# Kernel tuning notes

Measured on AMD Instinct MI355X. Metric: run time of the kernel, lower is better.

The kernel has to match this reference:

```python
import jax, jax.numpy as jnp
import numpy as np

NUM_HEADS = 8
WS = 8          # window_size
MO = 12         # (1 + overlap) * window_size
PAD = 2         # overlap * window_size / 2


def setup_inputs() -> dict:
    key = jax.random.key(0)
    ks = jax.random.split(key, 5)
    B, C, H, W = 16, 256, 64, 64
    x = jax.random.normal(ks[0], (B, C, H, W), jnp.float32)
    W1 = jax.random.normal(ks[1], (3 * C, C), jnp.float32) * 0.02
    b1 = jnp.zeros((3 * C,), jnp.float32)
    W2 = jax.random.normal(ks[2], (C, C), jnp.float32) * 0.02
    b2 = jnp.zeros((C,), jnp.float32)
    return {"x": x, "W1": W1, "b1": b1, "W2": W2, "b2": b2}


def _unfold_windows(t, nwin):
    # t: (B, H, W, C) -> overlapping windows (B, nH, nwin, nwin, MO*MO, E)
    # Matches torch nn.Unfold(kernel=MO, stride=WS, padding=PAD) layout:
    # channels outermost, then kernel rows, then kernel cols.
    B, H, W, C = t.shape
    E = C // NUM_HEADS
    p = jnp.pad(t.transpose(0, 3, 1, 2), ((0, 0), (0, 0), (PAD, PAD), (PAD, PAD)))
    idx = (jnp.arange(nwin) * WS)[:, None] + jnp.arange(MO)  # (nwin, MO)
    g = p[:, :, idx]            # (B, C, nwin, MO, Wp)
    g = g[:, :, :, :, idx]      # (B, C, nwin, MO, nwin, MO)
    g = g.transpose(0, 1, 2, 4, 3, 5)            # (B, C, nwin, nwin, MO, MO)
    g = g.reshape(B, NUM_HEADS, E, nwin, nwin, MO * MO)
    return g.transpose(0, 1, 3, 4, 5, 2)         # (B, nH, nwin, nwin, MO^2, E)


def reference(x, W1, b1, W2, b2):
    B, C, H, W = x.shape
    E = C // NUM_HEADS
    nwin = H // WS
    t = x.transpose(0, 2, 3, 1)                  # (B, H, W, C)
    qkv = t @ W1.T + b1                          # (B, H, W, 3C)
    # '(c K)' layout with K=3: channel index outer, K inner -> strided split
    Q = qkv[..., 0::3]
    K = qkv[..., 1::3]
    V = qkv[..., 2::3]
    # Q -> non-overlapping windows: (B, nH, nwin, nwin, WS^2, E)
    Qw = Q.reshape(B, nwin, WS, nwin, WS, NUM_HEADS, E)
    Qw = Qw.transpose(0, 5, 1, 3, 2, 4, 6).reshape(B, NUM_HEADS, nwin, nwin, WS * WS, E)
    Kw = _unfold_windows(K, nwin)
    Vw = _unfold_windows(V, nwin)
    scale = 1.0 / jnp.sqrt(jnp.float32(E))
    scores = jnp.einsum('bhijqe,bhijke->bhijqk', Qw, Kw) * scale  # (B,nH,nw,nw,WS^2,MO^2)
    A = jax.nn.softmax(scores, axis=-1)
    out = jnp.einsum('bhijqk,bhijke->bhijqe', A, Vw)              # (B,nH,nw,nw,WS^2,E)
    out = out.reshape(B, NUM_HEADS, nwin, nwin, WS, WS, E)
    out = out.transpose(0, 2, 4, 3, 5, 1, 6).reshape(B, H, W, C)
    y = out @ W2.T + b2                                           # (B, H, W, C)
    return y.transpose(0, 3, 1, 2)                                # (B, C, H, W)
```

## Files before the change

kernel.cpp:

```cpp
#include <hip/hip_runtime.h>
#include <stdint.h>

typedef unsigned short u16;
typedef unsigned int   u32;
typedef __bf16 bf16x8_t __attribute__((ext_vector_type(8)));
typedef float  f32x4_t  __attribute__((ext_vector_type(4)));

#define MFMA16(a, b, c) __builtin_amdgcn_mfma_f32_16x16x32_bf16((a), (b), (c), 0, 0, 0)

__device__ __forceinline__ float bf2f(u16 u) {
    union { u32 i; float f; } c; c.i = ((u32)u) << 16; return c.f;
}
__device__ __forceinline__ u16 f2bf(float f) {
    union { float f; u32 i; } c; c.f = f;
    u32 x = c.i;
    return (u16)((x + 0x7fffu + ((x >> 16) & 1u)) >> 16);
}
__device__ __forceinline__ u32 cvtpk(float lo, float hi) {
    u32 r;
    asm("v_cvt_pk_bf16_f32 %0, %1, %2" : "=v"(r) : "v"(lo), "v"(hi));
    return r;
}
__device__ __forceinline__ float exp2g(float x) {
    return __builtin_amdgcn_exp2f(x);
}

typedef const unsigned int __attribute__((address_space(1)))* gas_t;
typedef unsigned int __attribute__((address_space(3)))* las_t;
__device__ __forceinline__ void gload16(const u16* g, const u16* l) {
    __builtin_amdgcn_global_load_lds((gas_t)(const void*)g, (las_t)(void*)l, 16, 0, 0);
}

__device__ __forceinline__ u32 detect_fp32(const u16* __restrict__ xu,
                                           int tid, int* wcnt) {
    u16 w = xu[2 * tid];
    int e = (w >> 7) & 0xff;
    int ok = (e >= 80 && e <= 160) ? 1 : 0;
    unsigned long long m = __ballot(ok);
    if ((tid & 63) == 0) wcnt[tid >> 6] = __popcll(m);
    __syncthreads();
    int cnt = wcnt[0] + wcnt[1] + wcnt[2] + wcnt[3];
    return (cnt < 160) ? 1u : 0u;
}

__global__ __launch_bounds__(256) void conv_w(const u16* __restrict__ xu,
                                              const void* __restrict__ W1,
                                              const void* __restrict__ b1,
                                              const void* __restrict__ W2,
                                              const void* __restrict__ b2,
                                              u16* __restrict__ W1b,
                                              u16* __restrict__ b1b,
                                              u16* __restrict__ W2b,
                                              u16* __restrict__ b2b) {
    __shared__ int wcnt[4];
    u32 f = detect_fp32(xu, threadIdx.x, wcnt);
    int i = blockIdx.x * 256 + threadIdx.x;
    const int n1 = 196608, n2 = 768, n3 = 65536;
    if (i < n1) {
        int o = i >> 8, col = i & 255;
        int h = o / 96, rem = o - h * 96;
        int w = rem >> 5, e = rem & 31;
        int src = (3 * (h * 32 + e) + w) * 256 + col;
        W1b[i] = f ? f2bf(((const float*)W1)[src]) : ((const u16*)W1)[src];
    } else if (i < n1 + n2) {
        int o = i - n1;
        int h = o / 96, rem = o - h * 96;
        int w = rem >> 5, e = rem & 31;
        int src = 3 * (h * 32 + e) + w;
        b1b[o] = f ? f2bf(((const float*)b1)[src]) : ((const u16*)b1)[src];
    } else if (i < n1 + n2 + n3) {
        int li = i - n1 - n2;
        W2b[li] = f ? f2bf(((const float*)W2)[li]) : ((const u16*)W2)[li];
    } else {
        int li = i - n1 - n2 - n3;
        b2b[li] = f ? f2bf(((const float*)b2)[li]) : ((const u16*)b2)[li];
    }
}

__global__ __launch_bounds__(256) void conv_x(const void* __restrict__ X,
                                              u16* __restrict__ XT) {
    __shared__ __align__(16) u16 tile[64][68];
    __shared__ int wcnt[4];
    const int tid = threadIdx.x;
    u32 f = detect_fp32((const u16*)X, tid, wcnt);
    const int b = blockIdx.z, c0 = blockIdx.y * 64, h0 = blockIdx.x * 64;
    const int col = tid & 63, rq = tid >> 6;
    if (f) {
        const float* Xf = (const float*)X;
#pragma unroll
        for (int i = 0; i < 16; i++) {
            int row = i * 4 + rq;
            tile[row][col] = f2bf(Xf[((size_t)(b * 256 + c0 + row)) * 4096 + h0 + col]);
        }
    } else {
        const u16* Xh = (const u16*)X;
#pragma unroll
        for (int i = 0; i < 16; i++) {
            int row = i * 4 + rq;
            tile[row][col] = Xh[((size_t)(b * 256 + c0 + row)) * 4096 + h0 + col];
        }
    }
    __syncthreads();
#pragma unroll
    for (int i = 0; i < 16; i++) {
        int row = i * 4 + rq;
        XT[((size_t)(b * 4096 + h0 + row)) * 256 + c0 + col] = tile[col][row];
    }
}

__global__ __launch_bounds__(256) void gemm_qkv(const u16* __restrict__ XT,
                                                const u16* __restrict__ W1,
                                                const u16* __restrict__ b1,
                                                u16* __restrict__ Q2,
                                                u16* __restrict__ K2,
                                                u16* __restrict__ V2) {
    __shared__ __align__(16) u16 smem[128 * 64 + 96 * 64];
    u16* sA = smem;
    u16* sB = smem + 128 * 64;
    u16* Cs = smem;

    const int tid  = threadIdx.x;
    const int lane = tid & 63, wave = tid >> 6;
    const int quad = lane >> 4, l16 = lane & 15;
    const int wm = wave * 32;
    const int bx = blockIdx.x;
    const int bm = (bx >> 6) * 8 + (bx & 7);
    const int h  = (bx >> 3) & 7;
    const int o_base = h * 96;

    f32x4_t acc[2][6];
    const f32x4_t zz = {0.f, 0.f, 0.f, 0.f};
#pragma unroll
    for (int i = 0; i < 2; i++)
#pragma unroll
        for (int j = 0; j < 6; j++) acc[i][j] = zz;

    const int sub = lane >> 3;
    const int cpw = (lane & 7) ^ sub;
    const u16* gA[4]; const u16* gB[3];
    const u16* lA[4]; const u16* lB[3];
#pragma unroll
    for (int i = 0; i < 4; i++) {
        int r8 = (wave * 4 + i) * 8;
        gA[i] = XT + ((size_t)(bm * 128 + r8 + sub)) * 256 + cpw * 8;
        lA[i] = sA + r8 * 64;
    }
#pragma unroll
    for (int i = 0; i < 3; i++) {
        int r8 = (wave * 3 + i) * 8;
        gB[i] = W1 + ((size_t)(o_base + r8 + sub)) * 256 + cpw * 8;
        lB[i] = sB + r8 * 64;
    }

    for (int kt = 0; kt < 256; kt += 64) {
        __syncthreads();
#pragma unroll
        for (int i = 0; i < 4; i++) gload16(gA[i] + kt, lA[i]);
#pragma unroll
        for (int i = 0; i < 3; i++) gload16(gB[i] + kt, lB[i]);
        __syncthreads();
#pragma unroll
        for (int ks = 0; ks < 2; ks++) {
            bf16x8_t af[2], bg[6];
#pragma unroll
            for (int i = 0; i < 2; i++) {
                int row = wm + i * 16 + l16;
                int cp = (ks * 4 + quad) ^ (row & 7);
                af[i] = *(const bf16x8_t*)(sA + row * 64 + cp * 8);
            }
#pragma unroll
            for (int j = 0; j < 6; j++) {
                int row = j * 16 + l16;
                int cp = (ks * 4 + quad) ^ (row & 7);
                bg[j] = *(const bf16x8_t*)(sB + row * 64 + cp * 8);
            }
#pragma unroll
            for (int i = 0; i < 2; i++)
#pragma unroll
                for (int j = 0; j < 6; j++)
                    acc[i][j] = MFMA16(af[i], bg[j], acc[i][j]);
        }
    }

    __syncthreads();
#pragma unroll
    for (int j = 0; j < 6; j++) {
        float bias = bf2f(b1[o_base + j * 16 + l16]);
#pragma unroll
        for (int i = 0; i < 2; i++) {
            int m = wm + i * 16 + quad * 4;
#pragma unroll
            for (int r = 0; r < 4; r++)
                Cs[(m + r) * 104 + j * 16 + l16] = f2bf(acc[i][j][r] + bias);
        }
    }
    __syncthreads();

    const int b = bm >> 5;
    const int hw0 = (bm & 31) * 128;
    const size_t hb = ((size_t)(b * 8 + h)) * 4096;
#pragma unroll
    for (int it = 0; it < 2; it++) {
        int u = it * 256 + tid;
        int px = u >> 2, ch = u & 3;
        size_t gaddr = (hb + hw0 + px) * 32 + ch * 8;
        *(uint4*)(Q2 + gaddr) = *(const uint4*)(Cs + px * 104 +      ch * 8);
        *(uint4*)(K2 + gaddr) = *(const uint4*)(Cs + px * 104 + 32 + ch * 8);
        *(uint4*)(V2 + gaddr) = *(const uint4*)(Cs + px * 104 + 64 + ch * 8);
    }
}

__global__ __launch_bounds__(256) void attn_kernel(const u16* __restrict__ Q2,
                                                   const u16* __restrict__ K2,
                                                   const u16* __restrict__ V2,
                                                   u16* __restrict__ Op) {
    __shared__ __align__(16) u16 smem[16128];
    u16* Ks = smem;
    u16* Ps = smem;
    u16* Vt = smem + 10752;

    const int tid  = threadIdx.x;
    const int lane = tid & 63, wave = tid >> 6;
    const int quad = lane >> 4, l16 = lane & 15;
    const int win = blockIdx.x, head = blockIdx.y, b = blockIdx.z;
    const int wi = win >> 3, wj = win & 7;
    const size_t hb = ((size_t)(b * 8 + head)) * 4096;

    bf16x8_t aF;
    {
        int px = wave * 16 + l16;
        int qy = px >> 3, qx = px & 7;
        aF = *(const bf16x8_t*)(Q2 + (hb + (wi * 8 + qy) * 64 + wj * 8 + qx) * 32 + quad * 8);
    }
    for (int u = tid; u < 576; u += 256) {
        int px = u >> 2, ch = u & 3;
        int py = px / 12, kx = px - py * 12;
        int gy = wi * 8 - 2 + py, gx = wj * 8 - 2 + kx;
        uint4 kv = make_uint4(0, 0, 0, 0), vv = make_uint4(0, 0, 0, 0);
        if (gy >= 0 && gy < 64 && gx >= 0 && gx < 64) {
            size_t off = (hb + gy * 64 + gx) * 32 + ch * 8;
            kv = *(const uint4*)(K2 + off);
            vv = *(const uint4*)(V2 + off);
        }
        *(uint4*)(Ks + px * 40 + ch * 8) = kv;
        int colp = px ^ (ch << 3);
        int e0 = ch * 8;
        u32 w0[4] = {vv.x, vv.y, vv.z, vv.w};
#pragma unroll
        for (int p = 0; p < 4; p++) {
            Vt[(e0 + 2 * p    ) * 168 + colp] = (u16)(w0[p] & 0xffff);
            Vt[(e0 + 2 * p + 1) * 168 + colp] = (u16)(w0[p] >> 16);
        }
    }
    for (int t = tid; t < 512; t += 256) {
        int e = t >> 4, cl = 144 + (t & 15);
        Vt[e * 168 + (cl ^ ((e >> 3) << 3))] = 0;
    }
    __syncthreads();

    float s[9][4];
    {
        const f32x4_t zz = {0.f, 0.f, 0.f, 0.f};
#pragma unroll
        for (int j = 0; j < 9; j++) {
            bf16x8_t bF = *(const bf16x8_t*)(Ks + (j * 16 + l16) * 40 + quad * 8);
            f32x4_t d = MFMA16(aF, bF, zz);
#pragma unroll
            for (int r = 0; r < 4; r++) s[j][r] = d[r];
        }
    }
    float mx[4];
#pragma unroll
    for (int r = 0; r < 4; r++) {
        float a = fmaxf(fmaxf(s[0][r], s[1][r]), s[2][r]);
        a = fmaxf(fmaxf(a, s[3][r]), s[4][r]);
        a = fmaxf(fmaxf(a, s[5][r]), s[6][r]);
        a = fmaxf(fmaxf(a, s[7][r]), s[8][r]);
        mx[r] = a;
    }
#pragma unroll
    for (int off = 1; off < 16; off <<= 1)
#pragma unroll
        for (int r = 0; r < 4; r++) mx[r] = fmaxf(mx[r], __shfl_xor(mx[r], off, 16));

    __syncthreads();

    *(unsigned long long*)(Ps + (wave * 16 + l16) * 168 + 144 + quad * 4) = 0ULL;

    const float scale2 = 0.2550348632705143f;
    float msc[4];
#pragma unroll
    for (int r = 0; r < 4; r++) msc[r] = mx[r] * scale2;
    float sm[4] = {0.f, 0.f, 0.f, 0.f};
#pragma unroll
    for (int j = 0; j < 9; j++) {
        float p0 = exp2g(fmaf(s[j][0], scale2, -msc[0]));
        float p1 = exp2g(fmaf(s[j][1], scale2, -msc[1]));
        float p2 = exp2g(fmaf(s[j][2], scale2, -msc[2]));
        float p3 = exp2g(fmaf(s[j][3], scale2, -msc[3]));
        sm[0] += p0; sm[1] += p1; sm[2] += p2; sm[3] += p3;
        u32 a = cvtpk(p0, p1);
        u32 c = cvtpk(p2, p3);
        u16* base = Ps + (wave * 16 + quad * 4) * 168 + j * 16 + l16;
        base[0]   = (u16)a;
        base[168] = (u16)(a >> 16);
        base[336] = (u16)c;
        base[504] = (u16)(c >> 16);
    }
#pragma unroll
    for (int off = 1; off < 16; off <<= 1)
#pragma unroll
        for (int r = 0; r < 4; r++) sm[r] += __shfl_xor(sm[r], off, 16);

    __syncthreads();

    f32x4_t ob[2];
    ob[0] = (f32x4_t){0.f, 0.f, 0.f, 0.f};
    ob[1] = (f32x4_t){0.f, 0.f, 0.f, 0.f};
#pragma unroll
    for (int kk = 0; kk < 5; kk++) {
        bf16x8_t aP = *(const bf16x8_t*)(Ps + (wave * 16 + l16) * 168 + kk * 32 + quad * 8);
#pragma unroll
        for (int nt = 0; nt < 2; nt++) {
            int er = nt * 16 + l16;
            int sw = (er >> 3) << 3;
            bf16x8_t bV = *(const bf16x8_t*)(Vt + er * 168 + ((kk * 32 + quad * 8) ^ sw));
            ob[nt] = MFMA16(bV, aP, ob[nt]);
        }
    }
    {
        int srcl = (l16 >> 2) * 16;
        float d0 = __shfl(sm[0], srcl);
        float d1 = __shfl(sm[1], srcl);
        float d2 = __shfl(sm[2], srcl);
        float d3 = __shfl(sm[3], srcl);
        int rr = l16 & 3;
        float smq = (rr == 0) ? d0 : (rr == 1) ? d1 : (rr == 2) ? d2 : d3;
        float invq = 1.0f / smq;
        const int q = wave * 16 + l16;
        const int qy = q >> 3, qx = q & 7;
        const size_t obase =
            ((size_t)(b * 4096) + (wi * 8 + qy) * 64 + (wj * 8 + qx)) * 256 + head * 32;
#pragma unroll
        for (int nt = 0; nt < 2; nt++) {
            uint2 pk;
            pk.x = cvtpk(ob[nt][0] * invq, ob[nt][1] * invq);
            pk.y = cvtpk(ob[nt][2] * invq, ob[nt][3] * invq);
            *(uint2*)(Op + obase + nt * 16 + quad * 4) = pk;
        }
    }
}

__device__ __forceinline__ void gemm_loop(const u16* __restrict__ A,
                                          const u16* __restrict__ B,
                                          int K, int bm, int bn,
                                          u16* sA, u16* sB, f32x4_t acc[4][4]) {
    const int tid  = threadIdx.x;
    const int lane = tid & 63, wave = tid >> 6;
    const int quad = lane >> 4, l16 = lane & 15;
    const int wm = (wave >> 1) * 64, wn = (wave & 1) * 64;

    const int sub = lane >> 3;
    const int cpw = (lane & 7) ^ sub;
    const u16* gA[4]; const u16* gB[4];
    const u16* lA[4]; const u16* lB[4];
#pragma unroll
    for (int i = 0; i < 4; i++) {
        int r8 = (wave * 4 + i) * 8;
        gA[i] = A + ((size_t)(bm * 128 + r8 + sub)) * K + cpw * 8;
        gB[i] = B + ((size_t)(bn * 128 + r8 + sub)) * K + cpw * 8;
        lA[i] = sA + r8 * 64;
        lB[i] = sB + r8 * 64;
    }

    for (int kt = 0; kt < K; kt += 64) {
        __syncthreads();
#pragma unroll
        for (int i = 0; i < 4; i++) gload16(gA[i] + kt, lA[i]);
#pragma unroll
        for (int i = 0; i < 4; i++) gload16(gB[i] + kt, lB[i]);
        __syncthreads();
#pragma unroll
        for (int ks = 0; ks < 2; ks++) {
            bf16x8_t af[4], bg[4];
#pragma unroll
            for (int i = 0; i < 4; i++) {
                int row = wm + i * 16 + l16;
                int cp = (ks * 4 + quad) ^ (row & 7);
                af[i] = *(const bf16x8_t*)(sA + row * 64 + cp * 8);
            }
#pragma unroll
            for (int j = 0; j < 4; j++) {
                int row = wn + j * 16 + l16;
                int cp = (ks * 4 + quad) ^ (row & 7);
                bg[j] = *(const bf16x8_t*)(sB + row * 64 + cp * 8);
            }
#pragma unroll
            for (int i = 0; i < 4; i++)
#pragma unroll
                for (int j = 0; j < 4; j++)
                    acc[i][j] = MFMA16(af[i], bg[j], acc[i][j]);
        }
    }
}

__global__ __launch_bounds__(256) void gemm_out(const u16* __restrict__ xu,
                                                const u16* __restrict__ Ap,
                                                const u16* __restrict__ W2,
                                                const u16* __restrict__ b2,
                                                void* __restrict__ Y) {
    __shared__ __align__(16) u16 sA[128 * 64];
    __shared__ __align__(16) u16 sB[128 * 64];
    __shared__ int wcnt[4];
    const u32 out_f32 = detect_fp32(xu, threadIdx.x, wcnt);

    f32x4_t acc[4][4];
    const f32x4_t zz = {0.f, 0.f, 0.f, 0.f};
#pragma unroll
    for (int i = 0; i < 4; i++)
#pragma unroll
        for (int j = 0; j < 4; j++) acc[i][j] = zz;

    const int bm = blockIdx.x, bn = blockIdx.y;
    gemm_loop(Ap, W2, 256, bm, bn, sA, sB, acc);

    const int lane = threadIdx.x & 63, wave = threadIdx.x >> 6;
    const int quad = lane >> 4, l16 = lane & 15;
    const int wm = (wave >> 1) * 64, wn = (wave & 1) * 64;
    const int b = bm >> 5;
    const int hw0 = (bm & 31) * 128;
#pragma unroll
    for (int j = 0; j < 4; j++) {
        int o = bn * 128 + wn + j * 16 + l16;
        float bias = bf2f(b2[o]);
        size_t base = ((size_t)(b * 256 + o)) * 4096;
        if (out_f32) {
            float* Yf = (float*)Y;
#pragma unroll
            for (int i = 0; i < 4; i++) {
                int m0 = hw0 + wm + i * 16 + quad * 4;
                f32x4_t ov;
#pragma unroll
                for (int r = 0; r < 4; r++) ov[r] = acc[i][j][r] + bias;
                *(f32x4_t*)(Yf + base + m0) = ov;
            }
        } else {
            u16* Yh = (u16*)Y;
#pragma unroll
            for (int i = 0; i < 4; i++) {
                int m0 = hw0 + wm + i * 16 + quad * 4;
                uint2 pk;
                pk.x = cvtpk(acc[i][j][0] + bias, acc[i][j][1] + bias);
                pk.y = cvtpk(acc[i][j][2] + bias, acc[i][j][3] + bias);
                *(uint2*)(Yh + base + m0) = pk;
            }
        }
    }
}

extern "C" void kernel_launch(void* const* d_in, const int* in_sizes, int n_in,
                              void* d_out, int out_size, void* d_ws, size_t ws_size,
                              hipStream_t stream) {
    (void)in_sizes; (void)n_in; (void)out_size; (void)ws_size;
    const void* x  = d_in[0];
    const void* W1 = d_in[1];
    const void* b1 = d_in[2];
    const void* W2 = d_in[3];
    const void* b2 = d_in[4];
    const u16* xu = (const u16*)x;

    char* ws = (char*)d_ws;
    const size_t MB32 = (size_t)32 * 1024 * 1024;
    u16* xT  = (u16*)(ws);
    u16* Q2  = (u16*)(ws + MB32);
    u16* K2  = (u16*)(ws + 2 * MB32);
    u16* V2  = (u16*)(ws + 3 * MB32);
    u16* W1b = (u16*)(ws + 4 * MB32);
    u16* b1b = W1b + 196608;
    u16* W2b = b1b + 768;
    u16* b2b = W2b + 65536;
    u16* Op  = xT;

    conv_w  <<<1028, 256, 0, stream>>>(xu, W1, b1, W2, b2, W1b, b1b, W2b, b2b);
    conv_x  <<<dim3(64, 4, 16), 256, 0, stream>>>(x, xT);
    gemm_qkv<<<4096, 256, 0, stream>>>(xT, W1b, b1b, Q2, K2, V2);
    attn_kernel<<<dim3(64, 8, 16), 256, 0, stream>>>(Q2, K2, V2, Op);
    gemm_out<<<dim3(512, 2), 256, 0, stream>>>(xu, Op, W2b, b2b, d_out);
}
```

Before: 243.6 us.

## Keep softmax probabilities in registers via transposed QK MFMA and lane shuffles

Result: faster. 236.2 us (-3.0%).

```diff
diff --git a/kernel.cpp b/kernel.cpp
--- a/kernel.cpp
+++ b/kernel.cpp
@@ -210,14 +210,13 @@
     }
 }
 
-__global__ __launch_bounds__(256) void attn_kernel(const u16* __restrict__ Q2,
-                                                   const u16* __restrict__ K2,
-                                                   const u16* __restrict__ V2,
-                                                   u16* __restrict__ Op) {
-    __shared__ __align__(16) u16 smem[16128];
+__global__ __launch_bounds__(256, 6) void attn_kernel(const u16* __restrict__ Q2,
+                                                      const u16* __restrict__ K2,
+                                                      const u16* __restrict__ V2,
+                                                      u16* __restrict__ Op) {
+    __shared__ __align__(16) u16 smem[11136];
     u16* Ks = smem;
-    u16* Ps = smem;
-    u16* Vt = smem + 10752;
+    u16* Vt = smem + 5760;
 
     const int tid  = threadIdx.x;
     const int lane = tid & 63, wave = tid >> 6;
@@ -264,89 +263,81 @@
 #pragma unroll
         for (int j = 0; j < 9; j++) {
             bf16x8_t bF = *(const bf16x8_t*)(Ks + (j * 16 + l16) * 40 + quad * 8);
-            f32x4_t d = MFMA16(aF, bF, zz);
+            f32x4_t d = MFMA16(bF, aF, zz);
 #pragma unroll
             for (int r = 0; r < 4; r++) s[j][r] = d[r];
         }
     }
-    float mx[4];
-#pragma unroll
-    for (int r = 0; r < 4; r++) {
-        float a = fmaxf(fmaxf(s[0][r], s[1][r]), s[2][r]);
-        a = fmaxf(fmaxf(a, s[3][r]), s[4][r]);
-        a = fmaxf(fmaxf(a, s[5][r]), s[6][r]);
-        a = fmaxf(fmaxf(a, s[7][r]), s[8][r]);
-        mx[r] = a;
-    }
-#pragma unroll
-    for (int off = 1; off < 16; off <<= 1)
-#pragma unroll
-        for (int r = 0; r < 4; r++) mx[r] = fmaxf(mx[r], __shfl_xor(mx[r], off, 16));
-
-    __syncthreads();
-
-    *(unsigned long long*)(Ps + (wave * 16 + l16) * 168 + 144 + quad * 4) = 0ULL;
+    float mx;
+    {
+        float mj[9];
+#pragma unroll
+        for (int j = 0; j < 9; j++)
+            mj[j] = fmaxf(fmaxf(s[j][0], s[j][1]), fmaxf(s[j][2], s[j][3]));
+        float t0 = fmaxf(fmaxf(mj[0], mj[1]), fmaxf(mj[2], mj[3]));
+        float t1 = fmaxf(fmaxf(mj[4], mj[5]), fmaxf(mj[6], mj[7]));
+        mx = fmaxf(fmaxf(t0, t1), mj[8]);
+    }
+    mx = fmaxf(mx, __shfl_xor(mx, 16));
+    mx = fmaxf(mx, __shfl_xor(mx, 32));
 
     const float scale2 = 0.2550348632705143f;
-    float msc[4];
-#pragma unroll
-    for (int r = 0; r < 4; r++) msc[r] = mx[r] * scale2;
-    float sm[4] = {0.f, 0.f, 0.f, 0.f};
+    const float msc = mx * scale2;
+    float s0 = 0.f, s1 = 0.f, s2 = 0.f, s3 = 0.f;
+    u32 pk[9][2];
 #pragma unroll
     for (int j = 0; j < 9; j++) {
-        float p0 = exp2g(fmaf(s[j][0], scale2, -msc[0]));
-        float p1 = exp2g(fmaf(s[j][1], scale2, -msc[1]));
-        float p2 = exp2g(fmaf(s[j][2], scale2, -msc[2]));
-        float p3 = exp2g(fmaf(s[j][3], scale2, -msc[3]));
-        sm[0] += p0; sm[1] += p1; sm[2] += p2; sm[3] += p3;
-        u32 a = cvtpk(p0, p1);
-        u32 c = cvtpk(p2, p3);
-        u16* base = Ps + (wave * 16 + quad * 4) * 168 + j * 16 + l16;
-        base[0]   = (u16)a;
-        base[168] = (u16)(a >> 16);
-        base[336] = (u16)c;
-        base[504] = (u16)(c >> 16);
-    }
-#pragma unroll
-    for (int off = 1; off < 16; off <<= 1)
-#pragma unroll
-        for (int r = 0; r < 4; r++) sm[r] += __shfl_xor(sm[r], off, 16);
-
-    __syncthreads();
-
+        float p0 = exp2g(fmaf(s[j][0], scale2, -msc));
+        float p1 = exp2g(fmaf(s[j][1], scale2, -msc));
+        float p2 = exp2g(fmaf(s[j][2], scale2, -msc));
+        float p3 = exp2g(fmaf(s[j][3], scale2, -msc));
+        s0 += p0; s1 += p1; s2 += p2; s3 += p3;
+        pk[j][0] = cvtpk(p0, p1);
+        pk[j][1] = cvtpk(p2, p3);
+    }
+    float sm = (s0 + s1) + (s2 + s3);
+    sm += __shfl_xor(sm, 16);
+    sm += __shfl_xor(sm, 32);
+    const float invq = 1.0f / sm;
+
+    const int partA = (2 * (quad & 1)) * 16 + l16;
+    const int partB = partA + 16;
+    const bool hiQ = quad >= 2;
     f32x4_t ob[2];
     ob[0] = (f32x4_t){0.f, 0.f, 0.f, 0.f};
     ob[1] = (f32x4_t){0.f, 0.f, 0.f, 0.f};
 #pragma unroll
     for (int kk = 0; kk < 5; kk++) {
-        bf16x8_t aP = *(const bf16x8_t*)(Ps + (wave * 16 + l16) * 168 + kk * 32 + quad * 8);
+        const int jA = 2 * kk;
+        const int jB = (2 * kk + 1 > 8) ? 8 : 2 * kk + 1;
+        u32 a0 = __shfl(pk[jA][0], partA), b0 = __shfl(pk[jB][0], partA);
+        u32 a1 = __shfl(pk[jA][1], partA), b1 = __shfl(pk[jB][1], partA);
+        u32 a2 = __shfl(pk[jA][0], partB), b2 = __shfl(pk[jB][0], partB);
+        u32 a3 = __shfl(pk[jA][1], partB), b3 = __shfl(pk[jB][1], partB);
+        union { u32 u[4]; bf16x8_t v; } pb;
+        pb.u[0] = hiQ ? b0 : a0;
+        pb.u[1] = hiQ ? b1 : a1;
+        pb.u[2] = hiQ ? b2 : a2;
+        pb.u[3] = hiQ ? b3 : a3;
 #pragma unroll
         for (int nt = 0; nt < 2; nt++) {
             int er = nt * 16 + l16;
             int sw = (er >> 3) << 3;
             bf16x8_t bV = *(const bf16x8_t*)(Vt + er * 168 + ((kk * 32 + quad * 8) ^ sw));
-            ob[nt] = MFMA16(bV, aP, ob[nt]);
+            ob[nt] = MFMA16(bV, pb.v, ob[nt]);
         }
     }
     {
-        int srcl = (l16 >> 2) * 16;
-        float d0 = __shfl(sm[0], srcl);
-        float d1 = __shfl(sm[1], srcl);
-        float d2 = __shfl(sm[2], srcl);
-        float d3 = __shfl(sm[3], srcl);
-        int rr = l16 & 3;
-        float smq = (rr == 0) ? d0 : (rr == 1) ? d1 : (rr == 2) ? d2 : d3;
-        float invq = 1.0f / smq;
         const int q = wave * 16 + l16;
         const int qy = q >> 3, qx = q & 7;
         const size_t obase =
             ((size_t)(b * 4096) + (wi * 8 + qy) * 64 + (wj * 8 + qx)) * 256 + head * 32;
 #pragma unroll
         for (int nt = 0; nt < 2; nt++) {
-            uint2 pk;
-            pk.x = cvtpk(ob[nt][0] * invq, ob[nt][1] * invq);
-            pk.y = cvtpk(ob[nt][2] * invq, ob[nt][3] * invq);
-            *(uint2*)(Op + obase + nt * 16 + quad * 4) = pk;
+            uint2 pkk;
+            pkk.x = cvtpk(ob[nt][0] * invq, ob[nt][1] * invq);
+            pkk.y = cvtpk(ob[nt][2] * invq, ob[nt][3] * invq);
+            *(uint2*)(Op + obase + nt * 16 + quad * 4) = pkk;
         }
     }
 }
```
